# Kernel optimization log

Measured on AMD Instinct MI355X. Metric: run time of the kernel, lower is better.

The kernel has to match this reference:

```python
import jax, jax.numpy as jnp
import numpy as np

B, T, MAX_ITEMS = 128, 50, 32
NUM_PRODUCT, E, EW = 100000, 128, 16
D = E + EW  # rnn input/hidden size


def setup_inputs() -> dict:
    key = jax.random.key(0)
    ks = jax.random.split(key, 10)
    # items: 0 is padding; keep roughly half the slots padded (ragged baskets)
    items = jax.random.randint(ks[0], (B, T, MAX_ITEMS), 1, NUM_PRODUCT)
    keep = jax.random.uniform(ks[1], (B, T, MAX_ITEMS)) < 0.5
    keep = keep.at[:, :, 0].set(True)  # at least one item per basket
    items = jnp.where(keep, items, 0)
    flag = jax.random.randint(ks[2], (B, T, 1), 0, 2)
    x = jnp.concatenate([items, flag], axis=-1)  # [B,T,MAX_ITEMS+1], last col = flag
    lengths = jnp.full((B,), T, dtype=jnp.int64)
    hidden = jnp.zeros((1, B, D), dtype=jnp.float32)
    s_e = 1.0 / np.sqrt(E)
    s_d = 1.0 / np.sqrt(D)
    encode_w = jax.random.uniform(ks[3], (NUM_PRODUCT, E), minval=-0.1, maxval=0.1)
    encode_w = encode_w.at[0].set(0.0)  # padding_idx=0
    wchange_w = jax.random.normal(ks[4], (2, EW)) * 0.1
    wchange_w = wchange_w.at[0].set(0.0)  # padding_idx=0
    w_ih = jax.random.uniform(ks[5], (3 * D, D), minval=-s_d, maxval=s_d)
    w_hh = jax.random.uniform(ks[6], (3 * D, D), minval=-s_d, maxval=s_d)
    b_ih = jax.random.uniform(ks[7], (3 * D,), minval=-s_d, maxval=s_d)
    b_hh = jax.random.uniform(ks[8], (3 * D,), minval=-s_d, maxval=s_d)
    fc_w = jax.random.uniform(ks[9], (E, D), minval=-s_d, maxval=s_d)
    fc_b = jnp.zeros((E,), dtype=jnp.float32)
    return {"x": x, "lengths": lengths, "hidden": hidden,
            "encode_w": encode_w, "wchange_w": wchange_w,
            "w_ih": w_ih, "w_hh": w_hh, "b_ih": b_ih, "b_hh": b_hh,
            "fc_w": fc_w, "fc_b": fc_b}


def _embed_baskets(x, encode_w, wchange_w):
    items = x[..., :-1]                      # [B,T,I] product ids, 0 = pad
    flag = x[..., -1]                        # [B,T] 0/1 weight-change flag
    emb = encode_w[items]                    # [B,T,I,E] fused ragged gather
    mask = (items != 0).astype(emb.dtype)[..., None]
    cnt = jnp.maximum(mask.sum(axis=2), 1.0)
    pooled = (emb * mask).sum(axis=2) / cnt  # avg pool over real items [B,T,E]
    w = wchange_w[flag]                      # [B,T,EW]
    return jnp.concatenate([pooled, w], axis=-1)  # [B,T,D]


def _gru(seq, h0, w_ih, w_hh, b_ih, b_hh):
    # seq: [B,T,D], h0: [B,D]; torch GRU cell math
    def step(h, x_t):
        gi = x_t @ w_ih.T + b_ih             # [B,3D]
        gh = h @ w_hh.T + b_hh
        i_r, i_z, i_n = jnp.split(gi, 3, axis=-1)
        h_r, h_z, h_n = jnp.split(gh, 3, axis=-1)
        r = jax.nn.sigmoid(i_r + h_r)
        z = jax.nn.sigmoid(i_z + h_z)
        n = jnp.tanh(i_n + r * h_n)
        h_new = (1.0 - z) * n + z * h
        return h_new, h_new
    h_last, outs = jax.lax.scan(step, h0, jnp.swapaxes(seq, 0, 1))
    return jnp.swapaxes(outs, 0, 1), h_last  # [B,T,D], [B,D]


def reference(x, lengths, hidden, encode_w, wchange_w, w_ih, w_hh, b_ih, b_hh, fc_w, fc_b):
    seq = _embed_baskets(x, encode_w, wchange_w)         # [B,T,D]
    out, h_last = _gru(seq, hidden[0], w_ih, w_hh, b_ih, b_hh)
    dynamic_user = out @ fc_w.T + fc_b                   # [B,T,E]
    return dynamic_user, h_last[None]                    # h_u: [1,B,D]
```

## Files before the change

kernel.cpp:

```cpp
#include <hip/hip_runtime.h>
#include <math.h>

#define B_   128
#define T_   50
#define MI_  32
#define E_   128
#define EW_  16
#define D_   144
#define G_   432
#define N_   (B_*T_)

__global__ __launch_bounds__(128) void embed_kernel(
    const int* __restrict__ x,
    const float* __restrict__ encode_w,
    const float* __restrict__ wchange_w,
    float* __restrict__ seq)
{
    int n = blockIdx.x;
    int tid = threadIdx.x;
    __shared__ int xi[33];
    if (tid < 33) xi[tid] = x[n * 33 + tid];
    __syncthreads();

    float acc = 0.f;
    float cnt = 0.f;
    #pragma unroll
    for (int i = 0; i < MI_; ++i) {
        int it = xi[i];
        if (it != 0) {
            cnt += 1.f;
            acc += encode_w[it * E_ + tid];
        }
    }
    seq[n * D_ + tid] = acc / fmaxf(cnt, 1.f);
    if (tid < EW_) {
        int flag = xi[32];
        seq[n * D_ + E_ + tid] = wchange_w[flag * EW_ + tid];
    }
}

#define GK   144
#define GBK  48
#define GPAD 68

__global__ __launch_bounds__(256) void gemm_bias_kernel(
    const float* __restrict__ A,
    const float* __restrict__ Bw,
    const float* __restrict__ bias,
    float* __restrict__ C,
    int M, int N)
{
    __shared__ float As[GBK * GPAD];
    __shared__ float Bs[GBK * GPAD];

    int tid = threadIdx.x;
    int row0 = blockIdx.x * 64;
    int col0 = blockIdx.y * 64;
    int tx = tid & 15;
    int ty = tid >> 4;

    float acc[4][4] = {};

    int sr = tid >> 2;
    int skq0 = tid & 3;

    for (int k0 = 0; k0 < GK; k0 += GBK) {
        __syncthreads();
        #pragma unroll
        for (int i = 0; i < 3; ++i) {
            int kq = skq0 + i * 4;
            float4 a = *(const float4*)&A[(size_t)(row0 + sr) * GK + k0 + kq * 4];
            int nrow = col0 + sr;
            float4 b = make_float4(0.f, 0.f, 0.f, 0.f);
            if (nrow < N)
                b = *(const float4*)&Bw[(size_t)nrow * GK + k0 + kq * 4];
            As[(kq * 4 + 0) * GPAD + sr] = a.x;
            As[(kq * 4 + 1) * GPAD + sr] = a.y;
            As[(kq * 4 + 2) * GPAD + sr] = a.z;
            As[(kq * 4 + 3) * GPAD + sr] = a.w;
            Bs[(kq * 4 + 0) * GPAD + sr] = b.x;
            Bs[(kq * 4 + 1) * GPAD + sr] = b.y;
            Bs[(kq * 4 + 2) * GPAD + sr] = b.z;
            Bs[(kq * 4 + 3) * GPAD + sr] = b.w;
        }
        __syncthreads();

        #pragma unroll 4
        for (int k = 0; k < GBK; ++k) {
            float4 a4 = *(const float4*)&As[k * GPAD + ty * 4];
            float4 b4 = *(const float4*)&Bs[k * GPAD + tx * 4];
            float av[4] = {a4.x, a4.y, a4.z, a4.w};
            float bv[4] = {b4.x, b4.y, b4.z, b4.w};
            #pragma unroll
            for (int i = 0; i < 4; ++i)
                #pragma unroll
                for (int j = 0; j < 4; ++j)
                    acc[i][j] = fmaf(av[i], bv[j], acc[i][j]);
        }
    }

    int c = col0 + tx * 4;
    if (c < N) {
        float4 bb = *(const float4*)&bias[c];
        #pragma unroll
        for (int i = 0; i < 4; ++i) {
            int r = row0 + ty * 4 + i;
            float4 o;
            o.x = acc[i][0] + bb.x;
            o.y = acc[i][1] + bb.y;
            o.z = acc[i][2] + bb.z;
            o.w = acc[i][3] + bb.w;
            *(float4*)&C[(size_t)r * N + c] = o;
        }
    }
}

template<int CTRL>
__device__ __forceinline__ float dpp_xor_add(float x) {
    int y = __builtin_amdgcn_mov_dpp(__float_as_int(x), CTRL, 0xF, 0xF, true);
    return x + __int_as_float(y);
}

__global__ __launch_bounds__(576, 1) void gru_kernel(
    const float* __restrict__ gi,
    const float* __restrict__ w_hh,
    const float* __restrict__ b_hh,
    const float* __restrict__ h0,
    float* __restrict__ hseq,
    float* __restrict__ hlast)
{
    int b = blockIdx.x;
    int tid = threadIdx.x;
    int g = tid >> 3;
    int s = tid & 7;
    int k0 = s * 20;

    __shared__ __align__(16) float h[160];
    __shared__ float gh[G_];
    __shared__ __align__(16) float gilds[T_ * G_];
    __shared__ __align__(16) float hbuf[T_ * D_];

    {
        const float4* src = (const float4*)&gi[(size_t)b * T_ * G_];
        float4* dst = (float4*)gilds;
        for (int i = tid; i < (T_ * G_) / 4; i += 576) dst[i] = src[i];
    }

    float w[6][20];
    #pragma unroll
    for (int r = 0; r < 6; ++r) {
        const float* wrow = &w_hh[(size_t)(6 * g + r) * D_];
        #pragma unroll
        for (int q = 0; q < 5; ++q) {
            int k = k0 + 4 * q;
            float4 t = make_float4(0.f, 0.f, 0.f, 0.f);
            if (k < D_) t = *(const float4*)&wrow[k];
            w[r][4 * q + 0] = t.x;
            w[r][4 * q + 1] = t.y;
            w[r][4 * q + 2] = t.z;
            w[r][4 * q + 3] = t.w;
        }
    }
    float bias = (s < 6) ? b_hh[6 * g + s] : 0.f;

    if (tid < 160) h[tid] = (tid < D_) ? h0[b * D_ + tid] : 0.f;
    __syncthreads();

    for (int t = 0; t < T_; ++t) {
        float hv[20];
        #pragma unroll
        for (int q = 0; q < 5; ++q) {
            float4 t4 = *(const float4*)&h[k0 + 4 * q];
            hv[4 * q + 0] = t4.x;
            hv[4 * q + 1] = t4.y;
            hv[4 * q + 2] = t4.z;
            hv[4 * q + 3] = t4.w;
        }

        float a0 = 0.f, a1 = 0.f, a2 = 0.f, a3 = 0.f, a4 = 0.f, a5 = 0.f;
        #pragma unroll
        for (int kk = 0; kk < 20; ++kk) {
            float hk = hv[kk];
            a0 = fmaf(w[0][kk], hk, a0);
            a1 = fmaf(w[1][kk], hk, a1);
            a2 = fmaf(w[2][kk], hk, a2);
            a3 = fmaf(w[3][kk], hk, a3);
            a4 = fmaf(w[4][kk], hk, a4);
            a5 = fmaf(w[5][kk], hk, a5);
        }

        a0 = dpp_xor_add<0xB1>(a0); a0 = dpp_xor_add<0x4E>(a0); a0 = dpp_xor_add<0x141>(a0);
        a1 = dpp_xor_add<0xB1>(a1); a1 = dpp_xor_add<0x4E>(a1); a1 = dpp_xor_add<0x141>(a1);
        a2 = dpp_xor_add<0xB1>(a2); a2 = dpp_xor_add<0x4E>(a2); a2 = dpp_xor_add<0x141>(a2);
        a3 = dpp_xor_add<0xB1>(a3); a3 = dpp_xor_add<0x4E>(a3); a3 = dpp_xor_add<0x141>(a3);
        a4 = dpp_xor_add<0xB1>(a4); a4 = dpp_xor_add<0x4E>(a4); a4 = dpp_xor_add<0x141>(a4);
        a5 = dpp_xor_add<0xB1>(a5); a5 = dpp_xor_add<0x4E>(a5); a5 = dpp_xor_add<0x141>(a5);

        float myacc = a0;
        if (s == 1) myacc = a1;
        if (s == 2) myacc = a2;
        if (s == 3) myacc = a3;
        if (s == 4) myacc = a4;
        if (s == 5) myacc = a5;
        if (s < 6) gh[6 * g + s] = myacc + bias;
        __syncthreads();

        if (tid < D_) {
            float gir = gilds[t * G_ + tid];
            float giz = gilds[t * G_ + D_ + tid];
            float gin = gilds[t * G_ + 2 * D_ + tid];
            float r = 1.f / (1.f + __expf(-(gir + gh[tid])));
            float z = 1.f / (1.f + __expf(-(giz + gh[D_ + tid])));
            float narg = gin + r * gh[2 * D_ + tid];
            narg = fminf(fmaxf(narg, -15.f), 15.f);
            float e2 = __expf(-2.f * narg);
            float nn = (1.f - e2) / (1.f + e2);
            float hn = (1.f - z) * nn + z * h[tid];
            hbuf[t * D_ + tid] = hn;
            h[tid] = hn;
        }
        __syncthreads();
    }

    {
        const float4* src = (const float4*)hbuf;
        float4* dst = (float4*)&hseq[(size_t)b * T_ * D_];
        for (int i = tid; i < (T_ * D_) / 4; i += 576) dst[i] = src[i];
    }
    if (tid < D_) hlast[b * D_ + tid] = h[tid];
}

extern "C" void kernel_launch(void* const* d_in, const int* in_sizes, int n_in,
                              void* d_out, int out_size, void* d_ws, size_t ws_size,
                              hipStream_t stream)
{
    const int*   x         = (const int*)d_in[0];
    const float* hidden    = (const float*)d_in[2];
    const float* encode_w  = (const float*)d_in[3];
    const float* wchange_w = (const float*)d_in[4];
    const float* w_ih      = (const float*)d_in[5];
    const float* w_hh      = (const float*)d_in[6];
    const float* b_ih      = (const float*)d_in[7];
    const float* b_hh      = (const float*)d_in[8];
    const float* fc_w      = (const float*)d_in[9];
    const float* fc_b      = (const float*)d_in[10];

    float* out = (float*)d_out;
    float* ws  = (float*)d_ws;
    float* seq  = ws;
    float* gi   = ws + 921600;
    float* hseq = ws + 921600 + 2764800;

    embed_kernel<<<N_, 128, 0, stream>>>(x, encode_w, wchange_w, seq);

    gemm_bias_kernel<<<dim3(N_ / 64, (G_ + 63) / 64), 256, 0, stream>>>(
        seq, w_ih, b_ih, gi, N_, G_);

    gru_kernel<<<B_, 576, 0, stream>>>(gi, w_hh, b_hh, hidden, hseq,
                                       out + (size_t)N_ * E_);

    gemm_bias_kernel<<<dim3(N_ / 64, E_ / 64), 256, 0, stream>>>(
        hseq, fc_w, fc_b, out, N_, E_);
}
```

Measured before the change: 196.9 us.

## Fuse GRU gate math into dot-product lanes with double-buffered hidden state

Reassigns w_hh rows so each 8-lane group owns the r/z/n rows for two hidden units, letting the lanes that finish the DPP reduction apply the gate nonlinearity directly. This drops the shared gh array and one of the two barriers per timestep. Hidden state is ping-ponged between two LDS buffers to avoid the read/write race. gi is now read per step from global memory instead of being staged into LDS up front, which frees shared memory but puts global loads inside the serial loop (issued early to hide latency).

```diff
diff --git a/kernel.cpp b/kernel.cpp
--- a/kernel.cpp
+++ b/kernel.cpp
@@ -134,22 +134,19 @@
     int g = tid >> 3;
     int s = tid & 7;
     int k0 = s * 20;
-
-    __shared__ __align__(16) float h[160];
-    __shared__ float gh[G_];
-    __shared__ __align__(16) float gilds[T_ * G_];
+    int d0 = 2 * g;
+    int d  = d0 + (s & 1);
+    bool gate_lane = (s < 2);
+
+    __shared__ __align__(16) float hA[160];
+    __shared__ __align__(16) float hB[160];
     __shared__ __align__(16) float hbuf[T_ * D_];
 
-    {
-        const float4* src = (const float4*)&gi[(size_t)b * T_ * G_];
-        float4* dst = (float4*)gilds;
-        for (int i = tid; i < (T_ * G_) / 4; i += 576) dst[i] = src[i];
-    }
-
+    int rows[6] = {d0, d0 + 1, d0 + 144, d0 + 145, d0 + 288, d0 + 289};
     float w[6][20];
     #pragma unroll
     for (int r = 0; r < 6; ++r) {
-        const float* wrow = &w_hh[(size_t)(6 * g + r) * D_];
+        const float* wrow = &w_hh[(size_t)rows[r] * D_];
         #pragma unroll
         for (int q = 0; q < 5; ++q) {
             int k = k0 + 4 * q;
@@ -161,16 +158,36 @@
             w[r][4 * q + 3] = t.w;
         }
     }
-    float bias = (s < 6) ? b_hh[6 * g + s] : 0.f;
-
-    if (tid < 160) h[tid] = (tid < D_) ? h0[b * D_ + tid] : 0.f;
+    float br = 0.f, bz = 0.f, bn = 0.f;
+    if (gate_lane) {
+        br = b_hh[d];
+        bz = b_hh[d + D_];
+        bn = b_hh[d + 2 * D_];
+    }
+
+    if (tid < 160) {
+        hA[tid] = (tid < D_) ? h0[b * D_ + tid] : 0.f;
+        hB[tid] = 0.f;
+    }
     __syncthreads();
 
+    const float* gi_b = &gi[(size_t)b * T_ * G_];
+    float* hp = hA;
+    float* hq = hB;
+
     for (int t = 0; t < T_; ++t) {
+        float gir = 0.f, giz = 0.f, gin = 0.f, hold = 0.f;
+        if (gate_lane) {
+            gir  = gi_b[t * G_ + d];
+            giz  = gi_b[t * G_ + D_ + d];
+            gin  = gi_b[t * G_ + 2 * D_ + d];
+            hold = hp[d];
+        }
+
         float hv[20];
         #pragma unroll
         for (int q = 0; q < 5; ++q) {
-            float4 t4 = *(const float4*)&h[k0 + 4 * q];
+            float4 t4 = *(const float4*)&hp[k0 + 4 * q];
             hv[4 * q + 0] = t4.x;
             hv[4 * q + 1] = t4.y;
             hv[4 * q + 2] = t4.z;
@@ -196,30 +213,23 @@
         a4 = dpp_xor_add<0xB1>(a4); a4 = dpp_xor_add<0x4E>(a4); a4 = dpp_xor_add<0x141>(a4);
         a5 = dpp_xor_add<0xB1>(a5); a5 = dpp_xor_add<0x4E>(a5); a5 = dpp_xor_add<0x141>(a5);
 
-        float myacc = a0;
-        if (s == 1) myacc = a1;
-        if (s == 2) myacc = a2;
-        if (s == 3) myacc = a3;
-        if (s == 4) myacc = a4;
-        if (s == 5) myacc = a5;
-        if (s < 6) gh[6 * g + s] = myacc + bias;
-        __syncthreads();
-
-        if (tid < D_) {
-            float gir = gilds[t * G_ + tid];
-            float giz = gilds[t * G_ + D_ + tid];
-            float gin = gilds[t * G_ + 2 * D_ + tid];
-            float r = 1.f / (1.f + __expf(-(gir + gh[tid])));
-            float z = 1.f / (1.f + __expf(-(giz + gh[D_ + tid])));
-            float narg = gin + r * gh[2 * D_ + tid];
+        if (gate_lane) {
+            float ghr = (s == 0) ? a0 : a1;
+            float ghz = (s == 0) ? a2 : a3;
+            float ghn = (s == 0) ? a4 : a5;
+            float r = 1.f / (1.f + __expf(-(gir + ghr + br)));
+            float z = 1.f / (1.f + __expf(-(giz + ghz + bz)));
+            float narg = gin + r * (ghn + bn);
             narg = fminf(fmaxf(narg, -15.f), 15.f);
             float e2 = __expf(-2.f * narg);
             float nn = (1.f - e2) / (1.f + e2);
-            float hn = (1.f - z) * nn + z * h[tid];
-            hbuf[t * D_ + tid] = hn;
-            h[tid] = hn;
+            float hn = (1.f - z) * nn + z * hold;
+            hq[d] = hn;
+            hbuf[t * D_ + d] = hn;
         }
         __syncthreads();
+
+        float* tmp = hp; hp = hq; hq = tmp;
     }
 
     {
@@ -227,7 +237,7 @@
         float4* dst = (float4*)&hseq[(size_t)b * T_ * D_];
         for (int i = tid; i < (T_ * D_) / 4; i += 576) dst[i] = src[i];
     }
-    if (tid < D_) hlast[b * D_ + tid] = h[tid];
+    if (tid < D_) hlast[b * D_ + tid] = hp[tid];
 }
 
 extern "C" void kernel_launch(void* const* d_in, const int* in_sizes, int n_in,
```

Result: slower. 202.1 us (+2.7%).
